# Kernel optimization log

Measured on AMD Instinct MI355X. Metric: run time of the kernel, lower is better.

## Reference

```python
import jax, jax.numpy as jnp
import numpy as np

NUM_USERS = 100000
NUM_MOVIES = 50000
NUM_NODES = NUM_USERS + NUM_MOVIES
EMB_DIM = 64
N_LAYERS = 3
N_EDGES = 4000000


def setup_inputs() -> dict:
    key = jax.random.key(0)
    k_e, k_w = jax.random.split(key)
    edge_index = jax.random.randint(k_e, (2, N_EDGES), 0, NUM_NODES, dtype=jnp.int64 if jax.config.jax_enable_x64 else jnp.int32)
    emb_weight = jax.random.normal(k_w, (NUM_NODES, EMB_DIM), dtype=jnp.float32)
    return {"edge_index": edge_index, "emb_weight": emb_weight}


def reference(edge_index, emb_weight):
    row, col = edge_index[0], edge_index[1]
    num_nodes = emb_weight.shape[0]
    # degree of each node as a scatter-add destination (col)
    deg = jax.ops.segment_sum(jnp.ones_like(col, dtype=emb_weight.dtype), col,
                              num_segments=num_nodes)
    deg_inv_sqrt = jnp.where(deg > 0, jax.lax.rsqrt(jnp.maximum(deg, 1.0)), 0.0)
    deg_inv_sqrt = jnp.where(deg > 0, deg ** -0.5, 0.0)
    norm = deg_inv_sqrt[row] * deg_inv_sqrt[col]  # [E]

    embs = emb_weight
    acc = emb_weight  # running sum for the final mean over layers
    for _ in range(N_LAYERS):
        msgs = norm[:, None] * embs[row]  # [E, D] gather + scale
        embs = jax.ops.segment_sum(msgs, col, num_segments=num_nodes)  # [N, D]
        acc = acc + embs
    return acc / (N_LAYERS + 1)
```

## Files before the change

### kernel.cpp

```cpp
#include <hip/hip_runtime.h>
#include <hip/hip_fp16.h>

#define D 64
constexpr int TPB = 256;
constexpr int PTPB = 512;
constexpr int CTPB = 512;
constexpr int VSHIFT = 9;
constexpr int VNODES = 1 << VSHIFT;
constexpr int CHUNK = 16384;
typedef unsigned short u16;

__device__ inline unsigned h2pack(float a, float b) {
    unsigned lo = __half_as_ushort(__float2half_rn(a));
    unsigned hi = __half_as_ushort(__float2half_rn(b));
    return lo | (hi << 16);
}

__global__ void passA_kernel(const int* __restrict__ col, int* __restrict__ H,
                             int E, int NBLK, int NBUK) {
    __shared__ int h[VNODES];
    int t = threadIdx.x, blk = blockIdx.x;
    for (int b = t; b < NBUK; b += PTPB) h[b] = 0;
    __syncthreads();
    int base = blk * CHUNK, end = min(base + CHUNK, E);
    for (int i = base + t; i < end; i += PTPB)
        atomicAdd(&h[col[i] >> VSHIFT], 1);
    __syncthreads();
    for (int b = t; b < NBUK; b += PTPB) H[(size_t)b * NBLK + blk] = h[b];
}

__global__ void scan1_kernel(const int* __restrict__ v, int* __restrict__ part,
                             int* __restrict__ bsum, int M) {
    __shared__ int s[TPB];
    int t = threadIdx.x;
    int i = blockIdx.x * TPB + t;
    int x0 = (i < M) ? v[i] : 0;
    s[t] = x0;
    __syncthreads();
    for (int off = 1; off < TPB; off <<= 1) {
        int x = (t >= off) ? s[t - off] : 0;
        __syncthreads();
        s[t] += x;
        __syncthreads();
    }
    if (i < M) part[i] = s[t];
    if (t == TPB - 1) bsum[blockIdx.x] = s[t];
}

__global__ void scan2_kernel(const int* __restrict__ bsum, int* __restrict__ boff, int nb) {
    __shared__ int s[1024];
    int t = threadIdx.x;
    int v = (t < nb) ? bsum[t] : 0;
    s[t] = v;
    __syncthreads();
    for (int off = 1; off < 1024; off <<= 1) {
        int x = (t >= off) ? s[t - off] : 0;
        __syncthreads();
        s[t] += x;
        __syncthreads();
    }
    if (t < nb) boff[t] = s[t] - v;
}

__global__ void scan3_kernel(const int* __restrict__ v, const int* __restrict__ part,
                             const int* __restrict__ boff, int* __restrict__ pos, int M) {
    int i = blockIdx.x * blockDim.x + threadIdx.x;
    if (i < M) pos[i] = boff[blockIdx.x] + part[i] - v[i];
}

__global__ void passB_kernel(const int* __restrict__ row, const int* __restrict__ col,
                             const int* __restrict__ pos, unsigned* __restrict__ tmp,
                             int E, int NBLK, int NBUK) {
    __shared__ int cur[VNODES];
    int t = threadIdx.x, blk = blockIdx.x;
    for (int b = t; b < NBUK; b += PTPB) cur[b] = pos[(size_t)b * NBLK + blk];
    __syncthreads();
    int base = blk * CHUNK, end = min(base + CHUNK, E);
    for (int i = base + t; i < end; i += PTPB) {
        int c = col[i];
        int p = atomicAdd(&cur[c >> VSHIFT], 1);
        tmp[p] = ((unsigned)(c & (VNODES - 1)) << 18) | (unsigned)row[i];
    }
}

__global__ void passC_kernel(const unsigned* __restrict__ tmp, const int* __restrict__ pos,
                             int* __restrict__ row_ptr, float* __restrict__ dis,
                             int* __restrict__ srow,
                             const float2* __restrict__ emb2, unsigned* __restrict__ z,
                             unsigned* __restrict__ zb,
                             int N, int E, int NBLK, int NBUK) {
    __shared__ int cnt[VNODES], sc[VNODES], cur[VNODES];
    __shared__ int se[2];
    int b = blockIdx.x, t = threadIdx.x;
    int nodeBase = b << VSHIFT;
    if (t == 0) {
        se[0] = pos[(size_t)b * NBLK];
        se[1] = (b + 1 < NBUK) ? pos[(size_t)(b + 1) * NBLK] : E;
    }
    cnt[t] = 0;
    if (b == 0 && t < 32) {
        z[(size_t)N * 32 + t] = 0;
        zb[(size_t)N * 32 + t] = 0;
    }
    __syncthreads();
    int start = se[0], end = se[1];
    for (int i = start + t; i < end; i += CTPB)
        atomicAdd(&cnt[tmp[i] >> 18], 1);
    __syncthreads();
    sc[t] = cnt[t];
    __syncthreads();
    for (int off = 1; off < VNODES; off <<= 1) {
        int i = (t + 1) * (off << 1) - 1;
        if (i < VNODES) sc[i] += sc[i - off];
        __syncthreads();
    }
    if (t == 0) sc[VNODES - 1] = 0;
    __syncthreads();
    for (int off = VNODES / 2; off >= 1; off >>= 1) {
        int i = (t + 1) * (off << 1) - 1;
        if (i < VNODES) { int x = sc[i - off]; sc[i - off] = sc[i]; sc[i] += x; }
        __syncthreads();
    }
    {
        int rp = start + sc[t];
        cur[t] = rp;
        int node = nodeBase + t;
        if (node < N) {
            row_ptr[node] = rp;
            int d = cnt[t];
            dis[node] = (d > 0) ? rsqrtf((float)d) : 0.0f;
        }
    }
    if (b == 0 && t == 0) row_ptr[N] = E;
    __syncthreads();
    for (int i = start + t; i < end; i += CTPB) {
        unsigned pk = tmp[i];
        int p = atomicAdd(&cur[pk >> 18], 1);
        srow[p] = (int)(pk & 0x3FFFFu);
    }
    for (int i = t; i < (VNODES << 5); i += CTPB) {
        int k = i >> 5;
        int node = nodeBase + k;
        if (node < N) {
            int d = cnt[k];
            float dv = (d > 0) ? rsqrtf((float)d) : 0.0f;
            size_t o = (size_t)node * 32 + (i & 31);
            float2 x = emb2[o];
            z[o] = h2pack(dv * x.x, dv * x.y);
        }
    }
}

#define ACC8(u) do { \
    a0 += __half2float(__ushort_as_half((u16)((u).x & 0xffff))); \
    a1 += __half2float(__ushort_as_half((u16)((u).x >> 16)));    \
    a2 += __half2float(__ushort_as_half((u16)((u).y & 0xffff))); \
    a3 += __half2float(__ushort_as_half((u16)((u).y >> 16)));    \
    a4 += __half2float(__ushort_as_half((u16)((u).z & 0xffff))); \
    a5 += __half2float(__ushort_as_half((u16)((u).z >> 16)));    \
    a6 += __half2float(__ushort_as_half((u16)((u).w & 0xffff))); \
    a7 += __half2float(__ushort_as_half((u16)((u).w >> 16)));    \
} while (0)

template <int MODE, bool WRITE_DST>
__global__ void spmm_kernel(const int* __restrict__ row_ptr, const int* __restrict__ srow,
                            const float* __restrict__ dis,
                            const unsigned* __restrict__ src, unsigned* __restrict__ dst,
                            float2* __restrict__ out2, const float2* __restrict__ emb2,
                            int N) {
    int wave = (blockIdx.x * blockDim.x + threadIdx.x) >> 6;
    int lane = threadIdx.x & 63;
    int half = lane >> 5;
    int sub  = lane & 31;
    int node = 2 * wave + half;
    if (node >= N) return;
    int start = row_ptr[node];
    int end   = row_ptr[node + 1];
    int hb = half << 5;
    int rg = sub >> 3;
    int q  = sub & 7;
    const uint4* __restrict__ s4 = (const uint4*)src;
    float a0 = 0, a1 = 0, a2 = 0, a3 = 0, a4 = 0, a5 = 0, a6 = 0, a7 = 0;
    for (int base = start; base < end; base += 32) {
        int mye = base + sub;
        int rr = (mye < end) ? srow[mye] : 0;
        int cnt = end - base;
        int r0 = __shfl(rr, hb +  0 + rg);
        int r1 = __shfl(rr, hb +  4 + rg);
        int r2 = __shfl(rr, hb +  8 + rg);
        int r3 = __shfl(rr, hb + 12 + rg);
        int r4 = __shfl(rr, hb + 16 + rg);
        int r5 = __shfl(rr, hb + 20 + rg);
        int r6 = __shfl(rr, hb + 24 + rg);
        int r7 = __shfl(rr, hb + 28 + rg);
        r0 = ( 0 + rg < cnt) ? r0 : N;
        r1 = ( 4 + rg < cnt) ? r1 : N;
        r2 = ( 8 + rg < cnt) ? r2 : N;
        r3 = (12 + rg < cnt) ? r3 : N;
        r4 = (16 + rg < cnt) ? r4 : N;
        r5 = (20 + rg < cnt) ? r5 : N;
        r6 = (24 + rg < cnt) ? r6 : N;
        r7 = (28 + rg < cnt) ? r7 : N;
        uint4 u0 = s4[(size_t)r0 * 8 + q];
        uint4 u1 = s4[(size_t)r1 * 8 + q];
        uint4 u2 = s4[(size_t)r2 * 8 + q];
        uint4 u3 = s4[(size_t)r3 * 8 + q];
        uint4 u4 = s4[(size_t)r4 * 8 + q];
        uint4 u5 = s4[(size_t)r5 * 8 + q];
        uint4 u6 = s4[(size_t)r6 * 8 + q];
        uint4 u7 = s4[(size_t)r7 * 8 + q];
        ACC8(u0); ACC8(u1); ACC8(u2); ACC8(u3);
        ACC8(u4); ACC8(u5); ACC8(u6); ACC8(u7);
    }
    a0 += __shfl_xor(a0, 8);  a1 += __shfl_xor(a1, 8);
    a2 += __shfl_xor(a2, 8);  a3 += __shfl_xor(a3, 8);
    a4 += __shfl_xor(a4, 8);  a5 += __shfl_xor(a5, 8);
    a6 += __shfl_xor(a6, 8);  a7 += __shfl_xor(a7, 8);
    a0 += __shfl_xor(a0, 16); a1 += __shfl_xor(a1, 16);
    a2 += __shfl_xor(a2, 16); a3 += __shfl_xor(a3, 16);
    a4 += __shfl_xor(a4, 16); a5 += __shfl_xor(a5, 16);
    a6 += __shfl_xor(a6, 16); a7 += __shfl_xor(a7, 16);
    if (rg != 0) return;
    float dc = dis[node];
    float e0 = dc * a0, e1 = dc * a1, e2 = dc * a2, e3 = dc * a3;
    float e4 = dc * a4, e5 = dc * a5, e6 = dc * a6, e7 = dc * a7;
    if (WRITE_DST) {
        uint4 pk;
        pk.x = h2pack(dc * e0, dc * e1);
        pk.y = h2pack(dc * e2, dc * e3);
        pk.z = h2pack(dc * e4, dc * e5);
        pk.w = h2pack(dc * e6, dc * e7);
        ((uint4*)dst)[(size_t)node * 8 + q] = pk;
    }
    size_t fo = (size_t)node * 16 + q * 2;
    float4* __restrict__ o4 = (float4*)out2;
    float4 c0, c1;
    if (MODE == 0) {
        const float4* __restrict__ e4p = (const float4*)emb2;
        c0 = e4p[fo]; c1 = e4p[fo + 1];
        c0.x += e0; c0.y += e1; c0.z += e2; c0.w += e3;
        c1.x += e4; c1.y += e5; c1.z += e6; c1.w += e7;
    } else if (MODE == 1) {
        c0 = o4[fo]; c1 = o4[fo + 1];
        c0.x += e0; c0.y += e1; c0.z += e2; c0.w += e3;
        c1.x += e4; c1.y += e5; c1.z += e6; c1.w += e7;
    } else {
        c0 = o4[fo]; c1 = o4[fo + 1];
        c0.x = (c0.x + e0) * 0.25f; c0.y = (c0.y + e1) * 0.25f;
        c0.z = (c0.z + e2) * 0.25f; c0.w = (c0.w + e3) * 0.25f;
        c1.x = (c1.x + e4) * 0.25f; c1.y = (c1.y + e5) * 0.25f;
        c1.z = (c1.z + e6) * 0.25f; c1.w = (c1.w + e7) * 0.25f;
    }
    o4[fo] = c0; o4[fo + 1] = c1;
}

extern "C" void kernel_launch(void* const* d_in, const int* in_sizes, int n_in,
                              void* d_out, int out_size, void* d_ws, size_t ws_size,
                              hipStream_t stream) {
    const int* edge = (const int*)d_in[0];
    const float* emb = (const float*)d_in[1];
    const int E = in_sizes[0] / 2;
    const int N = in_sizes[1] / D;
    float2* out2 = (float2*)d_out;

    const int* row = edge;
    const int* col = edge + E;

    const int NBLK = (E + CHUNK - 1) / CHUNK;
    const int NBUK = (N + VNODES - 1) >> VSHIFT;
    const int M = NBUK * NBLK;
    const int nbH = (M + TPB - 1) / TPB;

    unsigned* A       = (unsigned*)d_ws;
    unsigned* B       = A + (size_t)(N + 1) * 32;
    int*      srow    = (int*)(B + (size_t)(N + 1) * 32);
    int*      row_ptr = srow + E;
    float*    dis     = (float*)(row_ptr + N + 1);
    int*      H       = (int*)(dis + N);
    int*      part    = H + M;
    int*      pos     = part + M;
    int*      bsum    = pos + M;
    int*      boff    = bsum + nbH;
    unsigned* tmp     = (unsigned*)(boff + nbH);

    const int spmm_blocks = (((N + 1) / 2) * 64 + TPB - 1) / TPB;

    passA_kernel<<<NBLK, PTPB, 0, stream>>>(col, H, E, NBLK, NBUK);
    scan1_kernel<<<nbH, TPB, 0, stream>>>(H, part, bsum, M);
    scan2_kernel<<<1, 1024, 0, stream>>>(bsum, boff, nbH);
    scan3_kernel<<<nbH, TPB, 0, stream>>>(H, part, boff, pos, M);
    passB_kernel<<<NBLK, PTPB, 0, stream>>>(row, col, pos, tmp, E, NBLK, NBUK);
    passC_kernel<<<NBUK, CTPB, 0, stream>>>(tmp, pos, row_ptr, dis, srow,
                                            (const float2*)emb, A, B, N, E, NBLK, NBUK);

    spmm_kernel<0, true><<<spmm_blocks, TPB, 0, stream>>>(row_ptr, srow, dis, A, B,
                                                          out2, (const float2*)emb, N);
    spmm_kernel<1, true><<<spmm_blocks, TPB, 0, stream>>>(row_ptr, srow, dis, B, A,
                                                          out2, (const float2*)emb, N);
    spmm_kernel<2, false><<<spmm_blocks, TPB, 0, stream>>>(row_ptr, srow, dis, A, nullptr,
                                                           out2, (const float2*)emb, N);
}
```

Baseline: 446.9 us.

## Replace two-level bucketed CSR build with global-atomic degree count and scatter

Replaces the bucketed radix-style CSR construction (per-block histograms, bucket scan, two scatter passes through a temp buffer) with a direct build. It counts degrees with global atomics, scans over nodes, then scatters row indices straight into srow using per-node atomic cursors. The scaled fp16 embedding init moves into its own grid-stride kernel. This cuts passes over the edge list and the temp buffer, but relies on 4M contended global atomics with random-address writes and gives a non-deterministic order of edges within each row.

New measurement: 794.8 us. 77.9% more time.

```diff
diff --git a/kernel.cpp b/kernel.cpp
--- a/kernel.cpp
+++ b/kernel.cpp
@@ -3,11 +3,6 @@
 
 #define D 64
 constexpr int TPB = 256;
-constexpr int PTPB = 512;
-constexpr int CTPB = 512;
-constexpr int VSHIFT = 9;
-constexpr int VNODES = 1 << VSHIFT;
-constexpr int CHUNK = 16384;
 typedef unsigned short u16;
 
 __device__ inline unsigned h2pack(float a, float b) {
@@ -16,17 +11,24 @@
     return lo | (hi << 16);
 }
 
-__global__ void passA_kernel(const int* __restrict__ col, int* __restrict__ H,
-                             int E, int NBLK, int NBUK) {
-    __shared__ int h[VNODES];
-    int t = threadIdx.x, blk = blockIdx.x;
-    for (int b = t; b < NBUK; b += PTPB) h[b] = 0;
-    __syncthreads();
-    int base = blk * CHUNK, end = min(base + CHUNK, E);
-    for (int i = base + t; i < end; i += PTPB)
-        atomicAdd(&h[col[i] >> VSHIFT], 1);
-    __syncthreads();
-    for (int b = t; b < NBUK; b += PTPB) H[(size_t)b * NBLK + blk] = h[b];
+__global__ void zero_kernel(int* __restrict__ deg, int N) {
+    int i = blockIdx.x * blockDim.x + threadIdx.x;
+    if (i < N) deg[i] = 0;
+}
+
+__global__ void deg_kernel(const int* __restrict__ col, int* __restrict__ deg,
+                           int E4, int E) {
+    const int4* __restrict__ c4 = (const int4*)col;
+    int stride = gridDim.x * blockDim.x;
+    for (int i = blockIdx.x * blockDim.x + threadIdx.x; i < E4; i += stride) {
+        int4 c = c4[i];
+        atomicAdd(&deg[c.x], 1);
+        atomicAdd(&deg[c.y], 1);
+        atomicAdd(&deg[c.z], 1);
+        atomicAdd(&deg[c.w], 1);
+    }
+    if (blockIdx.x == 0 && threadIdx.x < (E & 3))
+        atomicAdd(&deg[col[(E4 << 2) + threadIdx.x]], 1);
 }
 
 __global__ void scan1_kernel(const int* __restrict__ v, int* __restrict__ part,
@@ -62,92 +64,60 @@
     if (t < nb) boff[t] = s[t] - v;
 }
 
-__global__ void scan3_kernel(const int* __restrict__ v, const int* __restrict__ part,
-                             const int* __restrict__ boff, int* __restrict__ pos, int M) {
+__global__ void scan3c_kernel(const int* __restrict__ v, const int* __restrict__ part,
+                              const int* __restrict__ boff,
+                              int* __restrict__ row_ptr, int* __restrict__ cur,
+                              float* __restrict__ dis, int N, int E) {
     int i = blockIdx.x * blockDim.x + threadIdx.x;
-    if (i < M) pos[i] = boff[blockIdx.x] + part[i] - v[i];
-}
-
-__global__ void passB_kernel(const int* __restrict__ row, const int* __restrict__ col,
-                             const int* __restrict__ pos, unsigned* __restrict__ tmp,
-                             int E, int NBLK, int NBUK) {
-    __shared__ int cur[VNODES];
-    int t = threadIdx.x, blk = blockIdx.x;
-    for (int b = t; b < NBUK; b += PTPB) cur[b] = pos[(size_t)b * NBLK + blk];
-    __syncthreads();
-    int base = blk * CHUNK, end = min(base + CHUNK, E);
-    for (int i = base + t; i < end; i += PTPB) {
-        int c = col[i];
-        int p = atomicAdd(&cur[c >> VSHIFT], 1);
-        tmp[p] = ((unsigned)(c & (VNODES - 1)) << 18) | (unsigned)row[i];
-    }
-}
-
-__global__ void passC_kernel(const unsigned* __restrict__ tmp, const int* __restrict__ pos,
-                             int* __restrict__ row_ptr, float* __restrict__ dis,
-                             int* __restrict__ srow,
-                             const float2* __restrict__ emb2, unsigned* __restrict__ z,
-                             unsigned* __restrict__ zb,
-                             int N, int E, int NBLK, int NBUK) {
-    __shared__ int cnt[VNODES], sc[VNODES], cur[VNODES];
-    __shared__ int se[2];
-    int b = blockIdx.x, t = threadIdx.x;
-    int nodeBase = b << VSHIFT;
-    if (t == 0) {
-        se[0] = pos[(size_t)b * NBLK];
-        se[1] = (b + 1 < NBUK) ? pos[(size_t)(b + 1) * NBLK] : E;
-    }
-    cnt[t] = 0;
-    if (b == 0 && t < 32) {
-        z[(size_t)N * 32 + t] = 0;
-        zb[(size_t)N * 32 + t] = 0;
-    }
-    __syncthreads();
-    int start = se[0], end = se[1];
-    for (int i = start + t; i < end; i += CTPB)
-        atomicAdd(&cnt[tmp[i] >> 18], 1);
-    __syncthreads();
-    sc[t] = cnt[t];
-    __syncthreads();
-    for (int off = 1; off < VNODES; off <<= 1) {
-        int i = (t + 1) * (off << 1) - 1;
-        if (i < VNODES) sc[i] += sc[i - off];
-        __syncthreads();
-    }
-    if (t == 0) sc[VNODES - 1] = 0;
-    __syncthreads();
-    for (int off = VNODES / 2; off >= 1; off >>= 1) {
-        int i = (t + 1) * (off << 1) - 1;
-        if (i < VNODES) { int x = sc[i - off]; sc[i - off] = sc[i]; sc[i] += x; }
-        __syncthreads();
-    }
-    {
-        int rp = start + sc[t];
-        cur[t] = rp;
-        int node = nodeBase + t;
-        if (node < N) {
-            row_ptr[node] = rp;
-            int d = cnt[t];
-            dis[node] = (d > 0) ? rsqrtf((float)d) : 0.0f;
-        }
-    }
-    if (b == 0 && t == 0) row_ptr[N] = E;
-    __syncthreads();
-    for (int i = start + t; i < end; i += CTPB) {
-        unsigned pk = tmp[i];
-        int p = atomicAdd(&cur[pk >> 18], 1);
-        srow[p] = (int)(pk & 0x3FFFFu);
-    }
-    for (int i = t; i < (VNODES << 5); i += CTPB) {
-        int k = i >> 5;
-        int node = nodeBase + k;
-        if (node < N) {
-            int d = cnt[k];
-            float dv = (d > 0) ? rsqrtf((float)d) : 0.0f;
-            size_t o = (size_t)node * 32 + (i & 31);
-            float2 x = emb2[o];
-            z[o] = h2pack(dv * x.x, dv * x.y);
-        }
+    if (i < N) {
+        int ex = boff[blockIdx.x] + part[i] - v[i];
+        row_ptr[i] = ex;
+        cur[i] = ex;
+        int d = v[i];
+        dis[i] = (d > 0) ? rsqrtf((float)d) : 0.0f;
+    }
+    if (i == 0) row_ptr[N] = E;
+}
+
+__global__ void scatter_kernel(const int* __restrict__ row, const int* __restrict__ col,
+                               int* __restrict__ cur, int* __restrict__ srow,
+                               int E4, int E) {
+    const int4* __restrict__ c4 = (const int4*)col;
+    const int4* __restrict__ r4 = (const int4*)row;
+    int stride = gridDim.x * blockDim.x;
+    for (int i = blockIdx.x * blockDim.x + threadIdx.x; i < E4; i += stride) {
+        int4 c = c4[i];
+        int4 r = r4[i];
+        int p;
+        p = atomicAdd(&cur[c.x], 1); srow[p] = r.x;
+        p = atomicAdd(&cur[c.y], 1); srow[p] = r.y;
+        p = atomicAdd(&cur[c.z], 1); srow[p] = r.z;
+        p = atomicAdd(&cur[c.w], 1); srow[p] = r.w;
+    }
+    if (blockIdx.x == 0 && threadIdx.x < (E & 3)) {
+        int e = (E4 << 2) + threadIdx.x;
+        int p = atomicAdd(&cur[col[e]], 1);
+        srow[p] = row[e];
+    }
+}
+
+__global__ void z0_kernel(const float4* __restrict__ emb4, const float* __restrict__ dis,
+                          unsigned* __restrict__ A, unsigned* __restrict__ B, int N) {
+    int total = N * 16;
+    int stride = gridDim.x * blockDim.x;
+    uint2* __restrict__ A2 = (uint2*)A;
+    for (int i = blockIdx.x * blockDim.x + threadIdx.x; i < total; i += stride) {
+        int node = i >> 4;
+        float dv = dis[node];
+        float4 x = emb4[i];
+        uint2 o;
+        o.x = h2pack(dv * x.x, dv * x.y);
+        o.y = h2pack(dv * x.z, dv * x.w);
+        A2[i] = o;
+    }
+    if (blockIdx.x == 0 && threadIdx.x < 32) {
+        A[(size_t)N * 32 + threadIdx.x] = 0;
+        B[(size_t)N * 32 + threadIdx.x] = 0;
     }
 }
 
@@ -266,32 +236,29 @@
     const int* row = edge;
     const int* col = edge + E;
 
-    const int NBLK = (E + CHUNK - 1) / CHUNK;
-    const int NBUK = (N + VNODES - 1) >> VSHIFT;
-    const int M = NBUK * NBLK;
-    const int nbH = (M + TPB - 1) / TPB;
+    const int nbN = (N + TPB - 1) / TPB;
+    const int E4  = E >> 2;
 
     unsigned* A       = (unsigned*)d_ws;
     unsigned* B       = A + (size_t)(N + 1) * 32;
     int*      srow    = (int*)(B + (size_t)(N + 1) * 32);
     int*      row_ptr = srow + E;
     float*    dis     = (float*)(row_ptr + N + 1);
-    int*      H       = (int*)(dis + N);
-    int*      part    = H + M;
-    int*      pos     = part + M;
-    int*      bsum    = pos + M;
-    int*      boff    = bsum + nbH;
-    unsigned* tmp     = (unsigned*)(boff + nbH);
+    int*      deg     = (int*)(dis + N);
+    int*      cur     = deg + N;
+    int*      part    = cur + N;
+    int*      bsum    = part + N;
+    int*      boff    = bsum + 1024;
 
     const int spmm_blocks = (((N + 1) / 2) * 64 + TPB - 1) / TPB;
 
-    passA_kernel<<<NBLK, PTPB, 0, stream>>>(col, H, E, NBLK, NBUK);
-    scan1_kernel<<<nbH, TPB, 0, stream>>>(H, part, bsum, M);
-    scan2_kernel<<<1, 1024, 0, stream>>>(bsum, boff, nbH);
-    scan3_kernel<<<nbH, TPB, 0, stream>>>(H, part, boff, pos, M);
-    passB_kernel<<<NBLK, PTPB, 0, stream>>>(row, col, pos, tmp, E, NBLK, NBUK);
-    passC_kernel<<<NBUK, CTPB, 0, stream>>>(tmp, pos, row_ptr, dis, srow,
-                                            (const float2*)emb, A, B, N, E, NBLK, NBUK);
+    zero_kernel<<<nbN, TPB, 0, stream>>>(deg, N);
+    deg_kernel<<<2048, TPB, 0, stream>>>(col, deg, E4, E);
+    scan1_kernel<<<nbN, TPB, 0, stream>>>(deg, part, bsum, N);
+    scan2_kernel<<<1, 1024, 0, stream>>>(bsum, boff, nbN);
+    scan3c_kernel<<<nbN, TPB, 0, stream>>>(deg, part, boff, row_ptr, cur, dis, N, E);
+    scatter_kernel<<<2048, TPB, 0, stream>>>(row, col, cur, srow, E4, E);
+    z0_kernel<<<2048, TPB, 0, stream>>>((const float4*)emb, dis, A, B, N);
 
     spmm_kernel<0, true><<<spmm_blocks, TPB, 0, stream>>>(row_ptr, srow, dis, A, B,
                                                           out2, (const float2*)emb, N);
```
